# Optimization experiments

Measured on AMD Instinct MI355X. Metric: run time of the kernel, lower is better.

Reference implementation:

```python
import jax, jax.numpy as jnp
import numpy as np

N, K, D_IN, H = 8192, 8, 512, 512
SCALE = 0.02  # weight init scale


def setup_inputs() -> dict:
    key = jax.random.key(0)
    ks = jax.random.split(key, 12)
    inp = {
        "x": jax.random.normal(ks[0], (N, D_IN), jnp.float32),
        "child_h": jax.random.normal(ks[1], (N, K, H), jnp.float32),
        "child_c": jax.random.normal(ks[2], (N, K, H), jnp.float32),
    }
    names = ["i", "f", "o", "u"]
    for idx, g in enumerate(names):
        inp["W" + g] = jax.random.normal(ks[3 + idx], (D_IN, H), jnp.float32) * SCALE
        inp["bW" + g] = jnp.zeros((H,), jnp.float32)
        inp["U" + g] = jax.random.normal(ks[7 + idx], (H, H), jnp.float32) * SCALE
        inp["bU" + g] = jnp.zeros((H,), jnp.float32)
    return inp


def reference(x, child_h, child_c,
              Wi, bWi, Ui, bUi,
              Wf, bWf, Uf, bUf,
              Wo, bWo, Uo, bUo,
              Wu, bWu, Uu, bUu):
    # Child-Sum Tree-LSTM, batched over N nodes each with K children.
    h_sum = child_h.sum(axis=1)                                   # [N, H]
    i = jax.nn.sigmoid(x @ Wi + bWi + h_sum @ Ui + bUi)           # [N, H]
    o = jax.nn.sigmoid(x @ Wo + bWo + h_sum @ Uo + bUo)           # [N, H]
    u = jnp.tanh(x @ Wu + bWu + h_sum @ Uu + bUu)                 # [N, H]
    # Per-child forget gates: f_k = sigmoid(W_f x + U_f h_k)
    f = jax.nn.sigmoid((x @ Wf + bWf)[:, None, :]
                       + jnp.einsum('nkh,hg->nkg', child_h, Uf) + bUf)  # [N, K, H]
    c = i * u + (f * child_c).sum(axis=1)                         # [N, H]
    h = o * jnp.tanh(c)                                           # [N, H]
    return jnp.stack([h, c], axis=0)                              # [2, N, H]
```

## Files before the change

### kernel.cpp

```cpp
#include <hip/hip_runtime.h>
#include <hip/hip_bf16.h>


#define NN 8192
#define KCH 8
#define HH 512

typedef __attribute__((ext_vector_type(4))) float f32x4;
typedef __attribute__((ext_vector_type(8))) short short8;

#define WAITV(N) asm volatile("s_waitcnt vmcnt(" #N ")" ::: "memory")
#define BAR() __builtin_amdgcn_s_barrier()

__device__ inline unsigned short f2bf(float f) {
    union { float f; unsigned u; } v; v.f = f;
    unsigned r = v.u + 0x7FFFu + ((v.u >> 16) & 1u);
    return (unsigned short)(r >> 16);
}
__device__ inline float bf2f(unsigned short b) {
    union { unsigned u; float f; } v; v.u = ((unsigned)b) << 16;
    return v.f;
}
__device__ inline float sigm(float x) { return 1.f / (1.f + __expf(-x)); }
__device__ inline float tanh_pf(float x) { return 2.f / (1.f + __expf(-2.f * x)) - 1.f; }

__device__ __forceinline__ void gl16(const unsigned short* gsrc, unsigned short* ldst) {
    __builtin_amdgcn_global_load_lds(
        (const __attribute__((address_space(1))) unsigned int*)gsrc,
        (__attribute__((address_space(3))) unsigned int*)ldst,
        16, 0, 0);
}


__global__ void k_cvt(const float* __restrict__ in, unsigned short* __restrict__ outp) {
    int i = blockIdx.x * blockDim.x + threadIdx.x;
    float4 a = ((const float4*)in)[2 * i];
    float4 b = ((const float4*)in)[2 * i + 1];
    uint4 o;
    o.x = (unsigned)f2bf(a.x) | ((unsigned)f2bf(a.y) << 16);
    o.y = (unsigned)f2bf(a.z) | ((unsigned)f2bf(a.w) << 16);
    o.z = (unsigned)f2bf(b.x) | ((unsigned)f2bf(b.y) << 16);
    o.w = (unsigned)f2bf(b.z) | ((unsigned)f2bf(b.w) << 16);
    ((uint4*)outp)[i] = o;
}

__global__ void k_hsum(const float* __restrict__ ch, unsigned short* __restrict__ hs,
                       unsigned short* __restrict__ chb) {
    int i = blockIdx.x * blockDim.x + threadIdx.x;
    int n = i >> 7, h4 = i & 127;
    const float4* base = (const float4*)(ch + (size_t)n * KCH * HH) + h4;
    float4 s = {0.f, 0.f, 0.f, 0.f};
#pragma unroll
    for (int k = 0; k < KCH; ++k) {
        float4 v = base[(size_t)k * 128];
        s.x += v.x; s.y += v.y; s.z += v.z; s.w += v.w;
        if (chb) {
            unsigned long long pk = (unsigned long long)f2bf(v.x)
                | ((unsigned long long)f2bf(v.y) << 16)
                | ((unsigned long long)f2bf(v.z) << 32)
                | ((unsigned long long)f2bf(v.w) << 48);
            *(unsigned long long*)&chb[((size_t)n * KCH + k) * 512 + h4 * 4] = pk;
        }
    }
    unsigned long long pk = (unsigned long long)f2bf(s.x)
        | ((unsigned long long)f2bf(s.y) << 16)
        | ((unsigned long long)f2bf(s.z) << 32)
        | ((unsigned long long)f2bf(s.w) << 48);
    *(unsigned long long*)&hs[(size_t)i * 4] = pk;
}

struct P8 { const float* p[8]; };
__global__ void k_transpose_w(P8 wsrc, unsigned short* __restrict__ out) {
    __shared__ float tile[32][33];
    const float* W = wsrc.p[blockIdx.z];
    unsigned short* O = out + (size_t)blockIdx.z * 262144;
    int k0 = blockIdx.x * 32, c0 = blockIdx.y * 32;
    for (int r = threadIdx.y; r < 32; r += 8)
        tile[r][threadIdx.x] = W[(size_t)(k0 + r) * 512 + c0 + threadIdx.x];
    __syncthreads();
    for (int r = threadIdx.y; r < 32; r += 8)
        O[(size_t)(c0 + r) * 512 + k0 + threadIdx.x] = f2bf(tile[threadIdx.x][r]);
}

__global__ __launch_bounds__(256, 2) void k_gates(
    const unsigned short* __restrict__ xb,
    const unsigned short* __restrict__ hsb,
    const unsigned short* __restrict__ wT,
    const float* __restrict__ bWi, const float* __restrict__ bUi,
    const float* __restrict__ bWf,
    const float* __restrict__ bWo, const float* __restrict__ bUo,
    const float* __restrict__ bWu, const float* __restrict__ bUu,
    unsigned short* __restrict__ Pq,
    unsigned short* __restrict__ Oq,
    unsigned short* __restrict__ Fq)
{
    __shared__ unsigned short lds[2][12288];
    const int t = threadIdx.x, lane = t & 63, wid = t >> 6;
    const int wr = wid >> 1, wc = wid & 1;
    const int nid = (blockIdx.x & 7) * 64 + (blockIdx.x >> 3);
    const int r0 = (nid >> 3) * 128, c0 = (nid & 7) * 64;

    f32x4 acc_i[4][2] = {}; f32x4 acc_f[4][2] = {};
    f32x4 acc_o[4][2] = {}; f32x4 acc_u[4][2] = {};

    const int frow = lane & 15, fk = (lane >> 4) * 8;

    auto stage0 = [&](unsigned short* buf, int kq) {
        for (int c = wid; c < 24; c += 4) {
            if (c < 8)
                gl16(&xb[(size_t)(r0 + c * 16 + frow) * 512 + kq + fk], &buf[c * 512]);
            else {
                int d = c - 8;
                gl16(&wT[(size_t)(d >> 2) * 262144 + (size_t)(c0 + (d & 3) * 16 + frow) * 512 + kq + fk],
                     &buf[4096 + d * 512]);
            }
        }
    };
    auto stage1 = [&](unsigned short* buf, int kq) {
        for (int c = wid; c < 20; c += 4) {
            if (c < 8)
                gl16(&hsb[(size_t)(r0 + c * 16 + frow) * 512 + kq + fk], &buf[c * 512]);
            else {
                int d = c - 8;
                gl16(&wT[(size_t)(4 + (d >> 2)) * 262144 + (size_t)(c0 + (d & 3) * 16 + frow) * 512 + kq + fk],
                     &buf[4096 + d * 512]);
            }
        }
    };

    stage0(lds[0], 0);

#pragma unroll 1
    for (int kq = 0; kq < 512; kq += 32) {
        unsigned short* cur = lds[(kq >> 5) & 1];
        unsigned short* nxt = lds[((kq >> 5) & 1) ^ 1];
        BAR();
        if (kq < 480) { stage0(nxt, kq + 32); WAITV(6); }
        else          { stage1(nxt, 0);       WAITV(5); }
        BAR();
        short8 af[4];
#pragma unroll
        for (int m = 0; m < 4; ++m) af[m] = *(const short8*)&cur[(wr * 4 + m) * 512 + lane * 8];
#pragma unroll
        for (int p = 0; p < 4; ++p) {
            short8 b0 = *(const short8*)&cur[4096 + (p * 4 + wc * 2 + 0) * 512 + lane * 8];
            short8 b1 = *(const short8*)&cur[4096 + (p * 4 + wc * 2 + 1) * 512 + lane * 8];
#pragma unroll
            for (int m = 0; m < 4; ++m) {
                if (p == 0) {
                    acc_i[m][0] = __builtin_amdgcn_mfma_f32_16x16x32_bf16(af[m], b0, acc_i[m][0], 0, 0, 0);
                    acc_i[m][1] = __builtin_amdgcn_mfma_f32_16x16x32_bf16(af[m], b1, acc_i[m][1], 0, 0, 0);
                } else if (p == 1) {
                    acc_f[m][0] = __builtin_amdgcn_mfma_f32_16x16x32_bf16(af[m], b0, acc_f[m][0], 0, 0, 0);
                    acc_f[m][1] = __builtin_amdgcn_mfma_f32_16x16x32_bf16(af[m], b1, acc_f[m][1], 0, 0, 0);
                } else if (p == 2) {
                    acc_o[m][0] = __builtin_amdgcn_mfma_f32_16x16x32_bf16(af[m], b0, acc_o[m][0], 0, 0, 0);
                    acc_o[m][1] = __builtin_amdgcn_mfma_f32_16x16x32_bf16(af[m], b1, acc_o[m][1], 0, 0, 0);
                } else {
                    acc_u[m][0] = __builtin_amdgcn_mfma_f32_16x16x32_bf16(af[m], b0, acc_u[m][0], 0, 0, 0);
                    acc_u[m][1] = __builtin_amdgcn_mfma_f32_16x16x32_bf16(af[m], b1, acc_u[m][1], 0, 0, 0);
                }
            }
        }
    }
#pragma unroll 1
    for (int kq = 0; kq < 512; kq += 32) {
        unsigned short* cur = lds[(kq >> 5) & 1];
        unsigned short* nxt = lds[((kq >> 5) & 1) ^ 1];
        BAR();
        if (kq < 480) { stage1(nxt, kq + 32); WAITV(5); }
        else          { WAITV(0); }
        BAR();
        short8 af[4];
#pragma unroll
        for (int m = 0; m < 4; ++m) af[m] = *(const short8*)&cur[(wr * 4 + m) * 512 + lane * 8];
#pragma unroll
        for (int p = 0; p < 3; ++p) {
            short8 b0 = *(const short8*)&cur[4096 + (p * 4 + wc * 2 + 0) * 512 + lane * 8];
            short8 b1 = *(const short8*)&cur[4096 + (p * 4 + wc * 2 + 1) * 512 + lane * 8];
#pragma unroll
            for (int m = 0; m < 4; ++m) {
                if (p == 0) {
                    acc_i[m][0] = __builtin_amdgcn_mfma_f32_16x16x32_bf16(af[m], b0, acc_i[m][0], 0, 0, 0);
                    acc_i[m][1] = __builtin_amdgcn_mfma_f32_16x16x32_bf16(af[m], b1, acc_i[m][1], 0, 0, 0);
                } else if (p == 1) {
                    acc_o[m][0] = __builtin_amdgcn_mfma_f32_16x16x32_bf16(af[m], b0, acc_o[m][0], 0, 0, 0);
                    acc_o[m][1] = __builtin_amdgcn_mfma_f32_16x16x32_bf16(af[m], b1, acc_o[m][1], 0, 0, 0);
                } else {
                    acc_u[m][0] = __builtin_amdgcn_mfma_f32_16x16x32_bf16(af[m], b0, acc_u[m][0], 0, 0, 0);
                    acc_u[m][1] = __builtin_amdgcn_mfma_f32_16x16x32_bf16(af[m], b1, acc_u[m][1], 0, 0, 0);
                }
            }
        }
    }
#pragma unroll
    for (int m = 0; m < 4; ++m) {
#pragma unroll
        for (int n = 0; n < 2; ++n) {
            int col = c0 + wc * 32 + n * 16 + (lane & 15);
            float bi = bWi[col] + bUi[col];
            float bf = bWf[col];
            float bo = bWo[col] + bUo[col];
            float bu = bWu[col] + bUu[col];
#pragma unroll
            for (int r = 0; r < 4; ++r) {
                int row = r0 + wr * 64 + m * 16 + (lane >> 4) * 4 + r;
                size_t idx = (size_t)row * 512 + col;
                float vi = sigm(acc_i[m][n][r] + bi);
                float vu = tanh_pf(acc_u[m][n][r] + bu);
                Pq[idx] = f2bf(vi * vu);
                Oq[idx] = f2bf(sigm(acc_o[m][n][r] + bo));
                Fq[idx] = f2bf(acc_f[m][n][r] + bf);
            }
        }
    }
}

__global__ __launch_bounds__(512, 2) void k_fc2(
    const unsigned short* __restrict__ chb,
    const float* __restrict__ cc,
    const unsigned short* __restrict__ ufT,
    const float* __restrict__ bUf,
    const unsigned short* __restrict__ Pq,
    const unsigned short* __restrict__ Oq,
    const unsigned short* __restrict__ Fq,
    float* __restrict__ out)
{
    __shared__ unsigned short lds[2][18432];
    const int t = threadIdx.x, lane = t & 63, wid = t >> 6;
    const int wc = wid;
    const int r0c = blockIdx.x * 64;

    f32x4 acc[4][4] = {};
    const int frow = lane & 15, fk = (lane >> 4) * 8;

    auto stage = [&](unsigned short* buf, int kq) {
#pragma unroll
        for (int j = 0; j < 5; ++j) {
            int c = wid + j * 8;
            if (c < 36) {
                if (c < 4)
                    gl16(&chb[(size_t)(r0c + c * 16 + frow) * 512 + kq + fk], &buf[c * 512]);
                else
                    gl16(&ufT[(size_t)((c - 4) * 16 + frow) * 512 + kq + fk],
                         &buf[2048 + (c - 4) * 512]);
            }
        }
    };

    stage(lds[0], 0);

#pragma unroll 1
    for (int kq = 0; kq < 512; kq += 32) {
        unsigned short* cur = lds[(kq >> 5) & 1];
        unsigned short* nxt = lds[((kq >> 5) & 1) ^ 1];
        BAR();
        if (kq < 480) {
            stage(nxt, kq + 32);
            if (wid < 4) { WAITV(5); } else { WAITV(4); }
        } else {
            WAITV(0);
        }
        BAR();
        short8 af[4], bfr[4];
#pragma unroll
        for (int m = 0; m < 4; ++m) af[m] = *(const short8*)&cur[m * 512 + lane * 8];
#pragma unroll
        for (int n = 0; n < 4; ++n) bfr[n] = *(const short8*)&cur[2048 + (wc * 4 + n) * 512 + lane * 8];
#pragma unroll
        for (int m = 0; m < 4; ++m)
#pragma unroll
            for (int n = 0; n < 4; ++n)
                acc[m][n] = __builtin_amdgcn_mfma_f32_16x16x32_bf16(af[m], bfr[n], acc[m][n], 0, 0, 0);
    }

    const int g = lane >> 4;
    float bUfv[4];
#pragma unroll
    for (int n = 0; n < 4; ++n) bUfv[n] = bUf[wc * 64 + n * 16 + (lane & 15)];

#pragma unroll
    for (int m = 0; m < 4; ++m) {
        int node = (r0c >> 3) + 2 * m + (g >> 1);
#pragma unroll
        for (int n = 0; n < 4; ++n) {
            int col = wc * 64 + n * 16 + (lane & 15);
            size_t nidx = (size_t)node * 512 + col;
            float xf = bf2f(Fq[nidx]) + bUfv[n];
            float fcs = 0.f;
#pragma unroll
            for (int r = 0; r < 4; ++r) {
                int R = r0c + m * 16 + g * 4 + r;
                fcs += sigm(acc[m][n][r] + xf) * cc[(size_t)R * 512 + col];
            }
            fcs += __shfl_xor(fcs, 16);
            if ((g & 1) == 0) {
                float cv = bf2f(Pq[nidx]) + fcs;
                out[nidx] = bf2f(Oq[nidx]) * tanh_pf(cv);
                out[(size_t)NN * HH + nidx] = cv;
            }
        }
    }
}

__global__ __launch_bounds__(512, 2) void k_fc_fb(
    const float* __restrict__ ch, const float* __restrict__ cc,
    const unsigned short* __restrict__ ufT, const float* __restrict__ bUf,
    const unsigned short* __restrict__ Pq, const unsigned short* __restrict__ Oq,
    const unsigned short* __restrict__ Fq, float* __restrict__ out)
{
    __shared__ unsigned short lds[2][18432];
    const int t = threadIdx.x, lane = t & 63, wid = t >> 6;
    const int wc = wid;
    const int r0c = blockIdx.x * 64;
    f32x4 acc[4][4] = {};
    const int frow = lane & 15, fk = (lane >> 4) * 8;

    auto stage = [&](unsigned short* buf, int kq) {
        if (t < 256) {
            int row = 16 * (t >> 6) + (t & 15), ks = (t >> 4) & 3;
            const float* src = &ch[(size_t)(r0c + row) * 512 + kq + ks * 8];
            float4 v0 = *(const float4*)src;
            float4 v1 = *(const float4*)(src + 4);
            uint4 o;
            o.x = (unsigned)f2bf(v0.x) | ((unsigned)f2bf(v0.y) << 16);
            o.y = (unsigned)f2bf(v0.z) | ((unsigned)f2bf(v0.w) << 16);
            o.z = (unsigned)f2bf(v1.x) | ((unsigned)f2bf(v1.y) << 16);
            o.w = (unsigned)f2bf(v1.z) | ((unsigned)f2bf(v1.w) << 16);
            *(uint4*)&buf[t * 8] = o;
        } else {
            int w = wid - 4;
#pragma unroll
            for (int j = 0; j < 8; ++j)
                gl16(&ufT[(size_t)((w * 8 + j) * 16 + frow) * 512 + kq + fk],
                     &buf[2048 + (w * 8 + j) * 512]);
        }
    };

    stage(lds[0], 0);
#pragma unroll 1
    for (int kq = 0; kq < 512; kq += 32) {
        unsigned short* cur = lds[(kq >> 5) & 1];
        unsigned short* nxt = lds[((kq >> 5) & 1) ^ 1];
        __syncthreads();
        if (kq < 480) stage(nxt, kq + 32);
        short8 af[4], bfr[4];
#pragma unroll
        for (int m = 0; m < 4; ++m) af[m] = *(const short8*)&cur[m * 512 + lane * 8];
#pragma unroll
        for (int n = 0; n < 4; ++n) bfr[n] = *(const short8*)&cur[2048 + (wc * 4 + n) * 512 + lane * 8];
#pragma unroll
        for (int m = 0; m < 4; ++m)
#pragma unroll
            for (int n = 0; n < 4; ++n)
                acc[m][n] = __builtin_amdgcn_mfma_f32_16x16x32_bf16(af[m], bfr[n], acc[m][n], 0, 0, 0);
    }
    const int g = lane >> 4;
    float bUfv[4];
#pragma unroll
    for (int n = 0; n < 4; ++n) bUfv[n] = bUf[wc * 64 + n * 16 + (lane & 15)];
#pragma unroll
    for (int m = 0; m < 4; ++m) {
        int node = (r0c >> 3) + 2 * m + (g >> 1);
#pragma unroll
        for (int n = 0; n < 4; ++n) {
            int col = wc * 64 + n * 16 + (lane & 15);
            size_t nidx = (size_t)node * 512 + col;
            float xf = bf2f(Fq[nidx]) + bUfv[n];
            float fcs = 0.f;
#pragma unroll
            for (int r = 0; r < 4; ++r) {
                int R = r0c + m * 16 + g * 4 + r;
                fcs += sigm(acc[m][n][r] + xf) * cc[(size_t)R * 512 + col];
            }
            fcs += __shfl_xor(fcs, 16);
            if ((g & 1) == 0) {
                float cv = bf2f(Pq[nidx]) + fcs;
                out[nidx] = bf2f(Oq[nidx]) * tanh_pf(cv);
                out[(size_t)NN * HH + nidx] = cv;
            }
        }
    }
}

extern "C" void kernel_launch(void* const* d_in, const int* in_sizes, int n_in,
                              void* d_out, int out_size, void* d_ws, size_t ws_size,
                              hipStream_t stream) {
    const float* x   = (const float*)d_in[0];
    const float* ch  = (const float*)d_in[1];
    const float* cc  = (const float*)d_in[2];
    const float* Wi  = (const float*)d_in[3];  const float* bWi = (const float*)d_in[4];
    const float* Ui  = (const float*)d_in[5];  const float* bUi = (const float*)d_in[6];
    const float* Wf  = (const float*)d_in[7];  const float* bWf = (const float*)d_in[8];
    const float* Uf  = (const float*)d_in[9];  const float* bUf = (const float*)d_in[10];
    const float* Wo  = (const float*)d_in[11]; const float* bWo = (const float*)d_in[12];
    const float* Uo  = (const float*)d_in[13]; const float* bUo = (const float*)d_in[14];
    const float* Wu  = (const float*)d_in[15]; const float* bWu = (const float*)d_in[16];
    const float* Uu  = (const float*)d_in[17]; const float* bUu = (const float*)d_in[18];
    float* out = (float*)d_out;

    unsigned short* xb  = (unsigned short*)d_ws;
    unsigned short* hsb = xb  + (size_t)NN * HH;
    unsigned short* wT  = hsb + (size_t)NN * HH;
    unsigned short* Pq  = wT  + (size_t)8 * 262144;
    unsigned short* Oq  = Pq  + (size_t)NN * HH;
    unsigned short* Fq  = Oq  + (size_t)NN * HH;
    unsigned short* chb = Fq  + (size_t)NN * HH;

    size_t need = ((size_t)NN * HH * 5 + (size_t)8 * 262144 + (size_t)NN * KCH * HH) * 2;
    bool big = ws_size >= need;

    k_cvt<<<(NN * HH / 8) / 256, 256, 0, stream>>>(x, xb);
    k_hsum<<<(NN * 128) / 256, 256, 0, stream>>>(ch, hsb, big ? chb : nullptr);
    P8 wp;
    wp.p[0] = Wi; wp.p[1] = Wf; wp.p[2] = Wo; wp.p[3] = Wu;
    wp.p[4] = Ui; wp.p[5] = Uo; wp.p[6] = Uu; wp.p[7] = Uf;
    k_transpose_w<<<dim3(16, 16, 8), dim3(32, 8), 0, stream>>>(wp, wT);
    k_gates<<<dim3(512), 256, 0, stream>>>(xb, hsb, wT,
                                           bWi, bUi, bWf, bWo, bUo, bWu, bUu,
                                           Pq, Oq, Fq);
    if (big)
        k_fc2<<<dim3(1024), 512, 0, stream>>>(chb, cc, wT + (size_t)7 * 262144, bUf,
                                              Pq, Oq, Fq, out);
    else
        k_fc_fb<<<dim3(1024), 512, 0, stream>>>(ch, cc, wT + (size_t)7 * 262144, bUf,
                                                Pq, Oq, Fq, out);
}
```

Measured before the change: 217.0 us.

## Replace LDS-staged GEMM tiles with direct global-to-register fragment loads

Both the gate GEMM kernel and the forget-gate GEMM kernel drop LDS double buffering with barriers. Each wave now loads its MFMA fragments straight from global memory into registers. The forget kernel adds register double buffering and re-tiles to 256-thread blocks covering half the columns, doubling the grid. This removes barrier and LDS traffic but relies on the cache for operand reuse across waves, which may raise global load latency and duplicate fetches.

```diff
diff --git a/kernel.cpp b/kernel.cpp
--- a/kernel.cpp
+++ b/kernel.cpp
@@ -8,9 +8,6 @@
 
 typedef __attribute__((ext_vector_type(4))) float f32x4;
 typedef __attribute__((ext_vector_type(8))) short short8;
-
-#define WAITV(N) asm volatile("s_waitcnt vmcnt(" #N ")" ::: "memory")
-#define BAR() __builtin_amdgcn_s_barrier()
 
 __device__ inline unsigned short f2bf(float f) {
     union { float f; unsigned u; } v; v.f = f;
@@ -82,7 +79,16 @@
         O[(size_t)(c0 + r) * 512 + k0 + threadIdx.x] = f2bf(tile[threadIdx.x][r]);
 }
 
-__global__ __launch_bounds__(256, 2) void k_gates(
+__device__ __forceinline__ void gmm(f32x4 (&acc)[4][2], const short8 (&af)[4],
+                                    const short8 (&bq)[2]) {
+#pragma unroll
+    for (int m = 0; m < 4; ++m) {
+        acc[m][0] = __builtin_amdgcn_mfma_f32_16x16x32_bf16(af[m], bq[0], acc[m][0], 0, 0, 0);
+        acc[m][1] = __builtin_amdgcn_mfma_f32_16x16x32_bf16(af[m], bq[1], acc[m][1], 0, 0, 0);
+    }
+}
+
+__global__ __launch_bounds__(256) void k_gates_r(
     const unsigned short* __restrict__ xb,
     const unsigned short* __restrict__ hsb,
     const unsigned short* __restrict__ wT,
@@ -94,104 +100,46 @@
     unsigned short* __restrict__ Oq,
     unsigned short* __restrict__ Fq)
 {
-    __shared__ unsigned short lds[2][12288];
     const int t = threadIdx.x, lane = t & 63, wid = t >> 6;
     const int wr = wid >> 1, wc = wid & 1;
     const int nid = (blockIdx.x & 7) * 64 + (blockIdx.x >> 3);
     const int r0 = (nid >> 3) * 128, c0 = (nid & 7) * 64;
+    const int frow = lane & 15, fk = (lane >> 4) * 8;
+
+    const unsigned short* a0base = &xb[(size_t)(r0 + wr * 64 + frow) * 512 + fk];
+    const unsigned short* a1base = &hsb[(size_t)(r0 + wr * 64 + frow) * 512 + fk];
+    const unsigned short* bbase = &wT[(size_t)(c0 + wc * 32 + frow) * 512 + fk];
 
     f32x4 acc_i[4][2] = {}; f32x4 acc_f[4][2] = {};
     f32x4 acc_o[4][2] = {}; f32x4 acc_u[4][2] = {};
 
-    const int frow = lane & 15, fk = (lane >> 4) * 8;
-
-    auto stage0 = [&](unsigned short* buf, int kq) {
-        for (int c = wid; c < 24; c += 4) {
-            if (c < 8)
-                gl16(&xb[(size_t)(r0 + c * 16 + frow) * 512 + kq + fk], &buf[c * 512]);
-            else {
-                int d = c - 8;
-                gl16(&wT[(size_t)(d >> 2) * 262144 + (size_t)(c0 + (d & 3) * 16 + frow) * 512 + kq + fk],
-                     &buf[4096 + d * 512]);
-            }
-        }
-    };
-    auto stage1 = [&](unsigned short* buf, int kq) {
-        for (int c = wid; c < 20; c += 4) {
-            if (c < 8)
-                gl16(&hsb[(size_t)(r0 + c * 16 + frow) * 512 + kq + fk], &buf[c * 512]);
-            else {
-                int d = c - 8;
-                gl16(&wT[(size_t)(4 + (d >> 2)) * 262144 + (size_t)(c0 + (d & 3) * 16 + frow) * 512 + kq + fk],
-                     &buf[4096 + d * 512]);
-            }
-        }
-    };
-
-    stage0(lds[0], 0);
-
 #pragma unroll 1
     for (int kq = 0; kq < 512; kq += 32) {
-        unsigned short* cur = lds[(kq >> 5) & 1];
-        unsigned short* nxt = lds[((kq >> 5) & 1) ^ 1];
-        BAR();
-        if (kq < 480) { stage0(nxt, kq + 32); WAITV(6); }
-        else          { stage1(nxt, 0);       WAITV(5); }
-        BAR();
-        short8 af[4];
-#pragma unroll
-        for (int m = 0; m < 4; ++m) af[m] = *(const short8*)&cur[(wr * 4 + m) * 512 + lane * 8];
-#pragma unroll
-        for (int p = 0; p < 4; ++p) {
-            short8 b0 = *(const short8*)&cur[4096 + (p * 4 + wc * 2 + 0) * 512 + lane * 8];
-            short8 b1 = *(const short8*)&cur[4096 + (p * 4 + wc * 2 + 1) * 512 + lane * 8];
-#pragma unroll
-            for (int m = 0; m < 4; ++m) {
-                if (p == 0) {
-                    acc_i[m][0] = __builtin_amdgcn_mfma_f32_16x16x32_bf16(af[m], b0, acc_i[m][0], 0, 0, 0);
-                    acc_i[m][1] = __builtin_amdgcn_mfma_f32_16x16x32_bf16(af[m], b1, acc_i[m][1], 0, 0, 0);
-                } else if (p == 1) {
-                    acc_f[m][0] = __builtin_amdgcn_mfma_f32_16x16x32_bf16(af[m], b0, acc_f[m][0], 0, 0, 0);
-                    acc_f[m][1] = __builtin_amdgcn_mfma_f32_16x16x32_bf16(af[m], b1, acc_f[m][1], 0, 0, 0);
-                } else if (p == 2) {
-                    acc_o[m][0] = __builtin_amdgcn_mfma_f32_16x16x32_bf16(af[m], b0, acc_o[m][0], 0, 0, 0);
-                    acc_o[m][1] = __builtin_amdgcn_mfma_f32_16x16x32_bf16(af[m], b1, acc_o[m][1], 0, 0, 0);
-                } else {
-                    acc_u[m][0] = __builtin_amdgcn_mfma_f32_16x16x32_bf16(af[m], b0, acc_u[m][0], 0, 0, 0);
-                    acc_u[m][1] = __builtin_amdgcn_mfma_f32_16x16x32_bf16(af[m], b1, acc_u[m][1], 0, 0, 0);
-                }
-            }
-        }
+        short8 af[4], b0[2], b1[2], b2[2], b3[2];
+#pragma unroll
+        for (int m = 0; m < 4; ++m) af[m] = *(const short8*)(a0base + m * 8192 + kq);
+#pragma unroll
+        for (int q = 0; q < 2; ++q) {
+            b0[q] = *(const short8*)(bbase + 0 * 262144 + q * 8192 + kq);
+            b1[q] = *(const short8*)(bbase + 1 * 262144 + q * 8192 + kq);
+            b2[q] = *(const short8*)(bbase + 2 * 262144 + q * 8192 + kq);
+            b3[q] = *(const short8*)(bbase + 3 * 262144 + q * 8192 + kq);
+        }
+        gmm(acc_i, af, b0); gmm(acc_f, af, b1);
+        gmm(acc_o, af, b2); gmm(acc_u, af, b3);
     }
 #pragma unroll 1
     for (int kq = 0; kq < 512; kq += 32) {
-        unsigned short* cur = lds[(kq >> 5) & 1];
-        unsigned short* nxt = lds[((kq >> 5) & 1) ^ 1];
-        BAR();
-        if (kq < 480) { stage1(nxt, kq + 32); WAITV(5); }
-        else          { WAITV(0); }
-        BAR();
-        short8 af[4];
-#pragma unroll
-        for (int m = 0; m < 4; ++m) af[m] = *(const short8*)&cur[(wr * 4 + m) * 512 + lane * 8];
-#pragma unroll
-        for (int p = 0; p < 3; ++p) {
-            short8 b0 = *(const short8*)&cur[4096 + (p * 4 + wc * 2 + 0) * 512 + lane * 8];
-            short8 b1 = *(const short8*)&cur[4096 + (p * 4 + wc * 2 + 1) * 512 + lane * 8];
-#pragma unroll
-            for (int m = 0; m < 4; ++m) {
-                if (p == 0) {
-                    acc_i[m][0] = __builtin_amdgcn_mfma_f32_16x16x32_bf16(af[m], b0, acc_i[m][0], 0, 0, 0);
-                    acc_i[m][1] = __builtin_amdgcn_mfma_f32_16x16x32_bf16(af[m], b1, acc_i[m][1], 0, 0, 0);
-                } else if (p == 1) {
-                    acc_o[m][0] = __builtin_amdgcn_mfma_f32_16x16x32_bf16(af[m], b0, acc_o[m][0], 0, 0, 0);
-                    acc_o[m][1] = __builtin_amdgcn_mfma_f32_16x16x32_bf16(af[m], b1, acc_o[m][1], 0, 0, 0);
-                } else {
-                    acc_u[m][0] = __builtin_amdgcn_mfma_f32_16x16x32_bf16(af[m], b0, acc_u[m][0], 0, 0, 0);
-                    acc_u[m][1] = __builtin_amdgcn_mfma_f32_16x16x32_bf16(af[m], b1, acc_u[m][1], 0, 0, 0);
-                }
-            }
-        }
+        short8 af[4], b0[2], b1[2], b2[2];
+#pragma unroll
+        for (int m = 0; m < 4; ++m) af[m] = *(const short8*)(a1base + m * 8192 + kq);
+#pragma unroll
+        for (int q = 0; q < 2; ++q) {
+            b0[q] = *(const short8*)(bbase + 4 * 262144 + q * 8192 + kq);
+            b1[q] = *(const short8*)(bbase + 5 * 262144 + q * 8192 + kq);
+            b2[q] = *(const short8*)(bbase + 6 * 262144 + q * 8192 + kq);
+        }
+        gmm(acc_i, af, b0); gmm(acc_o, af, b1); gmm(acc_u, af, b2);
     }
 #pragma unroll
     for (int m = 0; m < 4; ++m) {
@@ -216,7 +164,7 @@
     }
 }
 
-__global__ __launch_bounds__(512, 2) void k_fc2(
+__global__ __launch_bounds__(256) void k_fc3(
     const unsigned short* __restrict__ chb,
     const float* __restrict__ cc,
     const unsigned short* __restrict__ ufT,
@@ -226,65 +174,50 @@
     const unsigned short* __restrict__ Fq,
     float* __restrict__ out)
 {
-    __shared__ unsigned short lds[2][18432];
-    const int t = threadIdx.x, lane = t & 63, wid = t >> 6;
-    const int wc = wid;
-    const int r0c = blockIdx.x * 64;
+    const int t = threadIdx.x, lane = t & 63, wc = t >> 6;
+    const int nid = (blockIdx.x & 7) * 256 + (blockIdx.x >> 3);
+    const int r0c = (nid >> 1) * 64;
+    const int c0 = (nid & 1) * 256;
+    const int frow = lane & 15, fk = (lane >> 4) * 8;
+
+    const unsigned short* abase = &chb[(size_t)(r0c + frow) * 512 + fk];
+    const unsigned short* bbase = &ufT[(size_t)(c0 + wc * 64 + frow) * 512 + fk];
 
     f32x4 acc[4][4] = {};
-    const int frow = lane & 15, fk = (lane >> 4) * 8;
-
-    auto stage = [&](unsigned short* buf, int kq) {
-#pragma unroll
-        for (int j = 0; j < 5; ++j) {
-            int c = wid + j * 8;
-            if (c < 36) {
-                if (c < 4)
-                    gl16(&chb[(size_t)(r0c + c * 16 + frow) * 512 + kq + fk], &buf[c * 512]);
-                else
-                    gl16(&ufT[(size_t)((c - 4) * 16 + frow) * 512 + kq + fk],
-                         &buf[2048 + (c - 4) * 512]);
-            }
-        }
-    };
-
-    stage(lds[0], 0);
-
+    short8 a0[4], b0[4], a1[4], b1[4];
+
+#define LDF(AS, BS, KQ) do { \
+    _Pragma("unroll") for (int m_ = 0; m_ < 4; ++m_) AS[m_] = *(const short8*)(abase + m_ * 8192 + (KQ)); \
+    _Pragma("unroll") for (int n_ = 0; n_ < 4; ++n_) BS[n_] = *(const short8*)(bbase + n_ * 8192 + (KQ)); \
+  } while (0)
+#define MMF(AS, BS) do { \
+    _Pragma("unroll") for (int m_ = 0; m_ < 4; ++m_) \
+    _Pragma("unroll") for (int n_ = 0; n_ < 4; ++n_) \
+        acc[m_][n_] = __builtin_amdgcn_mfma_f32_16x16x32_bf16(AS[m_], BS[n_], acc[m_][n_], 0, 0, 0); \
+  } while (0)
+
+    LDF(a0, b0, 0);
 #pragma unroll 1
-    for (int kq = 0; kq < 512; kq += 32) {
-        unsigned short* cur = lds[(kq >> 5) & 1];
-        unsigned short* nxt = lds[((kq >> 5) & 1) ^ 1];
-        BAR();
-        if (kq < 480) {
-            stage(nxt, kq + 32);
-            if (wid < 4) { WAITV(5); } else { WAITV(4); }
-        } else {
-            WAITV(0);
-        }
-        BAR();
-        short8 af[4], bfr[4];
-#pragma unroll
-        for (int m = 0; m < 4; ++m) af[m] = *(const short8*)&cur[m * 512 + lane * 8];
-#pragma unroll
-        for (int n = 0; n < 4; ++n) bfr[n] = *(const short8*)&cur[2048 + (wc * 4 + n) * 512 + lane * 8];
-#pragma unroll
-        for (int m = 0; m < 4; ++m)
-#pragma unroll
-            for (int n = 0; n < 4; ++n)
-                acc[m][n] = __builtin_amdgcn_mfma_f32_16x16x32_bf16(af[m], bfr[n], acc[m][n], 0, 0, 0);
-    }
+    for (int kq = 0; kq < 512; kq += 64) {
+        LDF(a1, b1, kq + 32);
+        MMF(a0, b0);
+        if (kq + 64 < 512) LDF(a0, b0, kq + 64);
+        MMF(a1, b1);
+    }
+#undef LDF
+#undef MMF
 
     const int g = lane >> 4;
     float bUfv[4];
 #pragma unroll
-    for (int n = 0; n < 4; ++n) bUfv[n] = bUf[wc * 64 + n * 16 + (lane & 15)];
+    for (int n = 0; n < 4; ++n) bUfv[n] = bUf[c0 + wc * 64 + n * 16 + (lane & 15)];
 
 #pragma unroll
     for (int m = 0; m < 4; ++m) {
         int node = (r0c >> 3) + 2 * m + (g >> 1);
 #pragma unroll
         for (int n = 0; n < 4; ++n) {
-            int col = wc * 64 + n * 16 + (lane & 15);
+            int col = c0 + wc * 64 + n * 16 + (lane & 15);
             size_t nidx = (size_t)node * 512 + col;
             float xf = bf2f(Fq[nidx]) + bUfv[n];
             float fcs = 0.f;
@@ -416,11 +349,11 @@
     wp.p[0] = Wi; wp.p[1] = Wf; wp.p[2] = Wo; wp.p[3] = Wu;
     wp.p[4] = Ui; wp.p[5] = Uo; wp.p[6] = Uu; wp.p[7] = Uf;
     k_transpose_w<<<dim3(16, 16, 8), dim3(32, 8), 0, stream>>>(wp, wT);
-    k_gates<<<dim3(512), 256, 0, stream>>>(xb, hsb, wT,
-                                           bWi, bUi, bWf, bWo, bUo, bWu, bUu,
-                                           Pq, Oq, Fq);
+    k_gates_r<<<dim3(512), 256, 0, stream>>>(xb, hsb, wT,
+                                             bWi, bUi, bWf, bWo, bUo, bWu, bUu,
+                                             Pq, Oq, Fq);
     if (big)
-        k_fc2<<<dim3(1024), 512, 0, stream>>>(chb, cc, wT + (size_t)7 * 262144, bUf,
+        k_fc3<<<dim3(2048), 256, 0, stream>>>(chb, cc, wT + (size_t)7 * 262144, bUf,
                                               Pq, Oq, Fq, out);
     else
         k_fc_fb<<<dim3(1024), 512, 0, stream>>>(ch, cc, wT + (size_t)7 * 262144, bUf,
```

Result: slower. 325.8 us (+50.2%).
